# Kernel tuning notes

Hardware: AMD Instinct MI355X
Metric: run time of the kernel (lower is better)

The kernel has to match this reference:

```python
import jax, jax.numpy as jnp
import numpy as np

INF = 1e9
EPS = 1e-5

def layer_norm(x, g, b):
    mu = jnp.mean(x, axis=-1, keepdims=True)
    var = jnp.mean(jnp.square(x - mu), axis=-1, keepdims=True)
    return (x - mu) * jax.lax.rsqrt(var + EPS) * g + b

def setup_inputs() -> dict:
    key = jax.random.key(0)
    ks = jax.random.split(key, 12)
    B, S, N = 1, 512, 384
    c_in, c_hid, c_z, H = 64, 32, 128, 8
    d = c_hid * H
    sc = lambda fan: 1.0 / np.sqrt(fan)
    return {
        "m": jax.random.normal(ks[0], (B, S, N, c_in), jnp.float32),
        "z": jax.random.normal(ks[1], (B, N, N, c_z), jnp.float32),
        "mask": jnp.ones((B, N, N), jnp.float32),
        "gamma_m": jnp.ones((c_in,), jnp.float32),
        "beta_m": jnp.zeros((c_in,), jnp.float32),
        "gamma_z": jnp.ones((c_z,), jnp.float32),
        "beta_z": jnp.zeros((c_z,), jnp.float32),
        "w_z": jax.random.normal(ks[2], (c_z, H), jnp.float32) * sc(c_z),
        "b_z": jnp.zeros((H,), jnp.float32),
        "w_v": jax.random.normal(ks[3], (c_in, d), jnp.float32) * sc(c_in),
        "b_v": jnp.zeros((d,), jnp.float32),
        "w_g": jax.random.normal(ks[4], (c_in, d), jnp.float32) * sc(c_in),
        "b_g": jnp.zeros((d,), jnp.float32),
        "w_o": jax.random.normal(ks[5], (d, c_in), jnp.float32) * sc(d),
        "b_o": jnp.zeros((c_in,), jnp.float32),
    }

def reference(m, z, mask, gamma_m, beta_m, gamma_z, beta_z,
              w_z, b_z, w_v, b_v, w_g, b_g, w_o, b_o):
    B, S, N, c_in = m.shape
    H = w_z.shape[-1]
    C = w_v.shape[-1] // H
    # pair branch: LN -> linear -> [B,H,Nq,Nk] logits + mask bias -> softmax
    zn = layer_norm(z, gamma_z, beta_z)
    logits = jnp.einsum('bqkz,zh->bhqk', zn, w_z) + b_z[None, :, None, None]
    logits = logits + (INF * (mask - 1.0))[:, None, :, :]
    w = jax.nn.softmax(logits, axis=-1)                      # [B,H,Nq,Nk]
    # MSA branch: LN -> value / gate projections
    mn = layer_norm(m, gamma_m, beta_m)
    v = (mn @ w_v + b_v).reshape(B, S, N, H, C)              # [B,S,Nk,H,C]
    o = jnp.einsum('bhqk,bskhc->bsqhc', w, v)                # broadcast over S
    g = jax.nn.sigmoid(mn @ w_g + b_g).reshape(B, S, N, H, C)
    out = (o * g).reshape(B, S, N, H * C) @ w_o + b_o
    return out
```

## Files before the change

### kernel.cpp

```cpp
#include <hip/hip_runtime.h>
#include <hip/hip_bf16.h>

#define INFV 1e9f
#define EPSV 1e-5f

typedef unsigned short u16;
typedef unsigned int u32;
typedef __attribute__((ext_vector_type(8))) short short8;
typedef __attribute__((ext_vector_type(4))) float float4v;

__device__ __forceinline__ u16 f2us(float f) {
    u32 v;
    __builtin_memcpy(&v, &f, 4);
    u32 r = v + 0x7fffu + ((v >> 16) & 1u);
    return (u16)(r >> 16);
}

__device__ __forceinline__ float wred_sum(float x) {
    #pragma unroll
    for (int o = 32; o; o >>= 1) x += __shfl_xor(x, o);
    return x;
}
__device__ __forceinline__ float wred_max(float x) {
    #pragma unroll
    for (int o = 32; o; o >>= 1) x = fmaxf(x, __shfl_xor(x, o));
    return x;
}

__global__ __launch_bounds__(256) void k_prep_ln(
    const float* __restrict__ m, const float* __restrict__ gm, const float* __restrict__ bm,
    u16* __restrict__ mn,
    const float* __restrict__ wv, const float* __restrict__ wg,
    const float* __restrict__ wo, const float* __restrict__ wz,
    u16* __restrict__ wv_t, u16* __restrict__ wg_t,
    u16* __restrict__ wo_t, u16* __restrict__ wzT)
{
    if (blockIdx.x < 12288) {
        const int tid  = threadIdx.x;
        const int wid  = tid >> 6;
        const int lane = tid & 63;
        const int rloc = lane >> 4;
        const int c4   = (lane & 15) * 4;
        const int row  = blockIdx.x * 16 + wid * 4 + rloc;
        const float4 x = *(const float4*)(m + (size_t)row * 64 + c4);
        float s1 = x.x + x.y + x.z + x.w;
        float s2 = x.x * x.x + x.y * x.y + x.z * x.z + x.w * x.w;
        #pragma unroll
        for (int o = 8; o; o >>= 1) { s1 += __shfl_xor(s1, o); s2 += __shfl_xor(s2, o); }
        const float mean = s1 * (1.0f / 64.0f);
        const float var  = s2 * (1.0f / 64.0f) - mean * mean;
        const float rs   = rsqrtf(var + EPSV);
        const float4 g = *(const float4*)(gm + c4);
        const float4 b = *(const float4*)(bm + c4);
        uint2 pk;
        pk.x = (u32)f2us((x.x - mean) * rs * g.x + b.x) | ((u32)f2us((x.y - mean) * rs * g.y + b.y) << 16);
        pk.y = (u32)f2us((x.z - mean) * rs * g.z + b.z) | ((u32)f2us((x.w - mean) * rs * g.w + b.w) << 16);
        *(uint2*)(mn + (size_t)row * 64 + c4) = pk;
    } else {
        const int i = (blockIdx.x - 12288) * 256 + threadIdx.x;
        if (i < 16384) {
            const int n = i >> 6, k = i & 63;
            wv_t[i] = f2us(wv[(size_t)k * 256 + n]);
        } else if (i < 32768) {
            const int j = i - 16384, n = j >> 6, k = j & 63;
            wg_t[j] = f2us(wg[(size_t)k * 256 + n]);
        } else if (i < 49152) {
            const int j = i - 32768, n = j >> 8, k = j & 255;
            wo_t[j] = f2us(wo[(size_t)k * 64 + n]);
        } else if (i < 51200) {
            const int j = i - 49152, n = j >> 7, k = j & 127;
            wzT[j] = (n < 8) ? f2us(wz[(size_t)k * 8 + n]) : (u16)0;
        }
    }
}

__global__ __launch_bounds__(256) void k_vT(
    const u16* __restrict__ mn, const u16* __restrict__ wv_t, u16* __restrict__ vTf)
{
    const int tid  = threadIdx.x;
    const int wid  = tid >> 6;
    const int lane = tid & 63;
    const int lrow = lane & 15;
    const int lkg  = lane >> 4;
    const int s    = blockIdx.y;
    const int k0   = blockIdx.x * 64 + wid * 16;

    const int kt   = blockIdx.x * 2 + (wid >> 1);
    const int lkgc = (wid & 1) * 2 + (lkg >> 1);
    const int joff = (lkg & 1) * 4;

    const u16* mnk = mn + ((size_t)s * 384 + k0 + lrow) * 64;
    const short8 a0 = *(const short8*)(mnk + lkg * 8);
    const short8 a1 = *(const short8*)(mnk + 32 + lkg * 8);

    #pragma unroll
    for (int nt = 0; nt < 16; nt++) {
        const short8 b0 = *(const short8*)(wv_t + (size_t)(nt * 16 + lrow) * 64 + lkg * 8);
        const short8 b1 = *(const short8*)(wv_t + (size_t)(nt * 16 + lrow) * 64 + 32 + lkg * 8);
        float4v acc = (float4v){0.f, 0.f, 0.f, 0.f};
        acc = __builtin_amdgcn_mfma_f32_16x16x32_bf16(a0, b0, acc, 0, 0, 0);
        acc = __builtin_amdgcn_mfma_f32_16x16x32_bf16(a1, b1, acc, 0, 0, 0);
        uint2 pk;
        pk.x = (u32)f2us(acc[0]) | ((u32)f2us(acc[1]) << 16);
        pk.y = (u32)f2us(acc[2]) | ((u32)f2us(acc[3]) << 16);
        *(uint2*)(vTf + ((((size_t)s * 12 + kt) * 16 + nt) << 9)
                      + ((lkgc << 4) + lrow) * 8 + joff) = pk;
    }
}

__global__ __launch_bounds__(256) void k_logits2(
    const float* __restrict__ z, const float* __restrict__ mask,
    const float* __restrict__ gz, const float* __restrict__ bz,
    const u16* __restrict__ wzT, const float* __restrict__ bzb,
    float* __restrict__ wbuf)
{
    const int tid   = threadIdx.x;
    const int wid   = tid >> 6;
    const int lane  = tid & 63;
    const int lrow  = lane & 15;
    const int lkg   = lane >> 4;
    const int pair0 = (blockIdx.x * 4 + wid) * 16;

    float x[4][8];
    float s1 = 0.0f, s2 = 0.0f;
    #pragma unroll
    for (int ks = 0; ks < 4; ks++) {
        const float4* zp = (const float4*)(z + (size_t)(pair0 + lrow) * 128 + ks * 32 + lkg * 8);
        const float4 a = zp[0], b = zp[1];
        x[ks][0] = a.x; x[ks][1] = a.y; x[ks][2] = a.z; x[ks][3] = a.w;
        x[ks][4] = b.x; x[ks][5] = b.y; x[ks][6] = b.z; x[ks][7] = b.w;
        #pragma unroll
        for (int j = 0; j < 8; j++) { s1 += x[ks][j]; s2 += x[ks][j] * x[ks][j]; }
    }
    s1 += __shfl_xor(s1, 16); s1 += __shfl_xor(s1, 32);
    s2 += __shfl_xor(s2, 16); s2 += __shfl_xor(s2, 32);
    const float mean = s1 * (1.0f / 128.0f);
    const float var  = s2 * (1.0f / 128.0f) - mean * mean;
    const float rs   = rsqrtf(var + EPSV);

    float4v acc = (float4v){0.f, 0.f, 0.f, 0.f};
    #pragma unroll
    for (int ks = 0; ks < 4; ks++) {
        const int c0 = ks * 32 + lkg * 8;
        const float4 g0 = *(const float4*)(gz + c0);
        const float4 g1 = *(const float4*)(gz + c0 + 4);
        const float4 b0 = *(const float4*)(bz + c0);
        const float4 b1 = *(const float4*)(bz + c0 + 4);
        const float gv[8] = {g0.x, g0.y, g0.z, g0.w, g1.x, g1.y, g1.z, g1.w};
        const float bvv[8] = {b0.x, b0.y, b0.z, b0.w, b1.x, b1.y, b1.z, b1.w};
        short8 afr;
        #pragma unroll
        for (int j = 0; j < 8; j++)
            afr[j] = (short)f2us((x[ks][j] - mean) * rs * gv[j] + bvv[j]);
        const short8 bfr = *(const short8*)(wzT + (size_t)lrow * 128 + c0);
        acc = __builtin_amdgcn_mfma_f32_16x16x32_bf16(afr, bfr, acc, 0, 0, 0);
    }
    if (lrow < 8) {
        const float bzv = bzb[lrow];
        #pragma unroll
        for (int r = 0; r < 4; r++) {
            const int p = pair0 + lkg * 4 + r;
            const float mb = INFV * (mask[p] - 1.0f);
            wbuf[(size_t)lrow * 147456 + p] = acc[r] + bzv + mb;
        }
    }
}

__global__ __launch_bounds__(256) void k_softmax_f(
    const float* __restrict__ wbuf, u16* __restrict__ wbf)
{
    const int r = blockIdx.x * 4 + (threadIdx.x >> 6);
    const int lane = threadIdx.x & 63;
    const float* base = wbuf + (size_t)r * 384;
    float v[6];
    float mx = -1e30f;
    #pragma unroll
    for (int j = 0; j < 6; j++) {
        v[j] = base[lane + j * 64];
        mx = fmaxf(mx, v[j]);
    }
    mx = wred_max(mx);
    float s = 0.0f;
    #pragma unroll
    for (int j = 0; j < 6; j++) {
        v[j] = __expf(v[j] - mx);
        s += v[j];
    }
    s = wred_sum(s);
    const float inv = 1.0f / s;

    const int h  = r / 384;
    const int q  = r - h * 384;
    const int qb = q >> 5;
    const int mt = (q >> 4) & 1;
    const int lr = q & 15;
    #pragma unroll
    for (int j = 0; j < 6; j++) {
        const int k   = lane + j * 64;
        const int kt  = k >> 5;
        const int lkg = (k >> 3) & 3;
        const int jj  = k & 7;
        wbf[((((size_t)(qb * 8 + h) * 12 + kt) * 2 + mt) << 9) + ((lkg << 4) + lr) * 8 + jj]
            = f2us(v[j] * inv);
    }
}

__global__ __launch_bounds__(256) void k_softmax(
    const float* __restrict__ wbuf, u16* __restrict__ wb16)
{
    const int r = blockIdx.x * 4 + (threadIdx.x >> 6);
    const int lane = threadIdx.x & 63;
    const float* base = wbuf + (size_t)r * 384;
    float v[6];
    float mx = -1e30f;
    #pragma unroll
    for (int j = 0; j < 6; j++) {
        v[j] = base[lane + j * 64];
        mx = fmaxf(mx, v[j]);
    }
    mx = wred_max(mx);
    float s = 0.0f;
    #pragma unroll
    for (int j = 0; j < 6; j++) {
        v[j] = __expf(v[j] - mx);
        s += v[j];
    }
    s = wred_sum(s);
    const float inv = 1.0f / s;
    u16* ob = wb16 + (size_t)r * 384;
    #pragma unroll
    for (int j = 0; j < 6; j++) ob[lane + j * 64] = f2us(v[j] * inv);
}

__global__ __launch_bounds__(512, 4) void k_fused7(
    const u16* __restrict__ mn, const u16* __restrict__ vTf,
    const float* __restrict__ bv, const float* __restrict__ bg, const float* __restrict__ bo,
    const u16* __restrict__ wg_t, const u16* __restrict__ wo_t,
    const u16* __restrict__ wbf, float* __restrict__ out)
{
    __shared__ __align__(16) u16 og[128 * 264];

    const int tid  = threadIdx.x;
    const int w    = tid >> 6;
    const int wq   = w >> 1;
    const int wh   = w & 1;
    const int lane = tid & 63;
    const int lrow = lane & 15;
    const int lkg  = lane >> 4;

    const int bid  = blockIdx.x;
    const int xcd  = bid & 7;
    const int slot = bid >> 3;
    const int sdiv = slot / 3;
    const int q0   = (slot - sdiv * 3) * 128;
    const int s    = sdiv * 8 + xcd;

    const int qb = (q0 >> 5) + wq;

    float4v oacc[16];
    #pragma unroll
    for (int mt = 0; mt < 2; mt++)
        #pragma unroll
        for (int nt = 0; nt < 8; nt++) {
            const float b = bv[wh * 128 + nt * 16 + lrow];
            oacc[mt * 8 + nt] = (float4v){b, b, b, b};
        }

    for (int kt = 0; kt < 12; kt++) {
        short8 bb[8];
        #pragma unroll
        for (int nt = 0; nt < 8; nt++) {
            const int ntg = wh * 8 + nt;
            bb[nt] = *(const short8*)(vTf + ((((size_t)s * 12 + kt) * 16 + ntg) << 9) + lane * 8);
        }
        #pragma unroll
        for (int hl = 0; hl < 4; hl++) {
            const int h = wh * 4 + hl;
            const size_t abase = (((size_t)(qb * 8 + h) * 12 + kt) * 2) << 9;
            const short8 a0 = *(const short8*)(wbf + abase + lane * 8);
            const short8 a1 = *(const short8*)(wbf + abase + 512 + lane * 8);
            #pragma unroll
            for (int sub = 0; sub < 2; sub++) {
                const int nt = hl * 2 + sub;
                oacc[nt]     = __builtin_amdgcn_mfma_f32_16x16x32_bf16(a0, bb[nt], oacc[nt], 0, 0, 0);
                oacc[8 + nt] = __builtin_amdgcn_mfma_f32_16x16x32_bf16(a1, bb[nt], oacc[8 + nt], 0, 0, 0);
            }
        }
    }

    {
        const u16* mnq = mn + ((size_t)s * 384 + q0 + wq * 32 + lrow) * 64;
        #pragma unroll
        for (int mt = 0; mt < 2; mt++) {
            const short8 a0 = *(const short8*)(mnq + mt * 1024 + lkg * 8);
            const short8 a1 = *(const short8*)(mnq + mt * 1024 + 32 + lkg * 8);
            #pragma unroll
            for (int nt = 0; nt < 8; nt++) {
                const int hc0 = wh * 128 + nt * 16;
                const float bgv = bg[hc0 + lrow];
                const short8 b0 = *(const short8*)(wg_t + (size_t)(hc0 + lrow) * 64 + lkg * 8);
                const short8 b1 = *(const short8*)(wg_t + (size_t)(hc0 + lrow) * 64 + 32 + lkg * 8);
                float4v gacc = (float4v){bgv, bgv, bgv, bgv};
                gacc = __builtin_amdgcn_mfma_f32_16x16x32_bf16(a0, b0, gacc, 0, 0, 0);
                gacc = __builtin_amdgcn_mfma_f32_16x16x32_bf16(a1, b1, gacc, 0, 0, 0);
                #pragma unroll
                for (int r = 0; r < 4; r++) {
                    const float sg = 1.0f / (1.0f + __expf(-gacc[r]));
                    og[(size_t)(wq * 32 + mt * 16 + lkg * 4 + r) * 264 + hc0 + lrow]
                        = f2us(oacc[mt * 8 + nt][r] * sg);
                }
            }
        }
    }
    __syncthreads();

    #pragma unroll
    for (int mt = 0; mt < 2; mt++) {
        short8 af[8];
        #pragma unroll
        for (int ks = 0; ks < 8; ks++)
            af[ks] = *(const short8*)&og[(size_t)(wq * 32 + mt * 16 + lrow) * 264 + ks * 32 + lkg * 8];
        #pragma unroll
        for (int ntl = 0; ntl < 2; ntl++) {
            const int nto = wh * 2 + ntl;
            const float bov = bo[nto * 16 + lrow];
            float4v fac = (float4v){bov, bov, bov, bov};
            #pragma unroll
            for (int ks = 0; ks < 8; ks++) {
                const short8 b = *(const short8*)(wo_t + (size_t)(nto * 16 + lrow) * 256 + ks * 32 + lkg * 8);
                fac = __builtin_amdgcn_mfma_f32_16x16x32_bf16(af[ks], b, fac, 0, 0, 0);
            }
            #pragma unroll
            for (int r = 0; r < 4; r++)
                out[((size_t)s * 384 + q0 + wq * 32 + mt * 16 + lkg * 4 + r) * 64 + nto * 16 + lrow]
                    = fac[r];
        }
    }
}

__global__ __launch_bounds__(256, 2) void k_fused4(
    const u16* __restrict__ mn,
    const float* __restrict__ bv, const float* __restrict__ bg, const float* __restrict__ bo,
    const u16* __restrict__ wv_t, const u16* __restrict__ wg_t, const u16* __restrict__ wo_t,
    const u16* __restrict__ wb16, float* __restrict__ out)
{
    __shared__ __align__(16) char smem[67584];
    u16* vtt = (u16*)smem;
    u16* og  = (u16*)smem;

    const int tid  = threadIdx.x;
    const int wid  = tid >> 6;
    const int lane = tid & 63;
    const int lrow = lane & 15;
    const int lkg  = lane >> 4;
    const int s    = blockIdx.y;
    const int q0   = blockIdx.x * 128;

    const int vmt  = wid & 1;
    const int vnt0 = (wid >> 1) * 8;

    float4v oacc[32];
    #pragma unroll
    for (int mt = 0; mt < 2; mt++)
        #pragma unroll
        for (int nt = 0; nt < 16; nt++) {
            const float b = bv[nt * 16 + lrow];
            oacc[mt * 16 + nt] = (float4v){b, b, b, b};
        }

    for (int kt = 0; kt < 12; kt++) {
        const int k0 = kt * 32;
        float4v vacc[8];
        #pragma unroll
        for (int nt = 0; nt < 8; nt++) vacc[nt] = (float4v){0.f, 0.f, 0.f, 0.f};
        const u16* mnk = mn + ((size_t)s * 384 + k0 + vmt * 16 + lrow) * 64;
        #pragma unroll
        for (int ks = 0; ks < 2; ks++) {
            const short8 a = *(const short8*)(mnk + ks * 32 + lkg * 8);
            #pragma unroll
            for (int nt = 0; nt < 8; nt++) {
                const short8 b = *(const short8*)(wv_t + (size_t)((vnt0 + nt) * 16 + lrow) * 64 + ks * 32 + lkg * 8);
                vacc[nt] = __builtin_amdgcn_mfma_f32_16x16x32_bf16(a, b, vacc[nt], 0, 0, 0);
            }
        }
        u16* vb = vtt + (size_t)(kt & 1) * 8192;
        const int kg8 = vmt * 2 + (lkg >> 1);
        const int ko  = (lkg & 1) * 4;
        #pragma unroll
        for (int nt = 0; nt < 8; nt++) {
            uint2 pk;
            pk.x = (u32)f2us(vacc[nt][0]) | ((u32)f2us(vacc[nt][1]) << 16);
            pk.y = (u32)f2us(vacc[nt][2]) | ((u32)f2us(vacc[nt][3]) << 16);
            *(uint2*)&vb[((size_t)kg8 * 256 + (vnt0 + nt) * 16 + lrow) * 8 + ko] = pk;
        }
        __syncthreads();

        short8 ah[2][8];
        #pragma unroll
        for (int mt = 0; mt < 2; mt++)
            #pragma unroll
            for (int h = 0; h < 8; h++)
                ah[mt][h] = *(const short8*)(wb16 + (size_t)h * 147456
                              + (size_t)(q0 + wid * 32 + mt * 16 + lrow) * 384 + k0 + lkg * 8);
        #pragma unroll
        for (int nt = 0; nt < 16; nt++) {
            const short8 b = *(const short8*)&vb[((size_t)lkg * 256 + nt * 16 + lrow) * 8];
            oacc[nt]      = __builtin_amdgcn_mfma_f32_16x16x32_bf16(ah[0][nt >> 1], b, oacc[nt], 0, 0, 0);
            oacc[16 + nt] = __builtin_amdgcn_mfma_f32_16x16x32_bf16(ah[1][nt >> 1], b, oacc[16 + nt], 0, 0, 0);
        }
    }
    __syncthreads();

    #pragma unroll
    for (int mt = 0; mt < 2; mt++) {
        const u16* mnq = mn + ((size_t)s * 384 + q0 + wid * 32 + mt * 16 + lrow) * 64;
        const short8 a0 = *(const short8*)(mnq + lkg * 8);
        const short8 a1 = *(const short8*)(mnq + 32 + lkg * 8);
        #pragma unroll
        for (int nt = 0; nt < 16; nt++) {
            const float bgv = bg[nt * 16 + lrow];
            float4v gacc = (float4v){bgv, bgv, bgv, bgv};
            const short8 b0 = *(const short8*)(wg_t + (size_t)(nt * 16 + lrow) * 64 + lkg * 8);
            const short8 b1 = *(const short8*)(wg_t + (size_t)(nt * 16 + lrow) * 64 + 32 + lkg * 8);
            gacc = __builtin_amdgcn_mfma_f32_16x16x32_bf16(a0, b0, gacc, 0, 0, 0);
            gacc = __builtin_amdgcn_mfma_f32_16x16x32_bf16(a1, b1, gacc, 0, 0, 0);
            #pragma unroll
            for (int r = 0; r < 4; r++) {
                const float sg = 1.0f / (1.0f + __expf(-gacc[r]));
                og[(size_t)(wid * 32 + mt * 16 + lkg * 4 + r) * 264 + nt * 16 + lrow]
                    = f2us(oacc[mt * 16 + nt][r] * sg);
            }
        }
    }
    __syncthreads();

    #pragma unroll
    for (int mt = 0; mt < 2; mt++) {
        short8 af[8];
        #pragma unroll
        for (int ks = 0; ks < 8; ks++)
            af[ks] = *(const short8*)&og[(size_t)(wid * 32 + mt * 16 + lrow) * 264 + ks * 32 + lkg * 8];
        #pragma unroll
        for (int nt = 0; nt < 4; nt++) {
            const float bov = bo[nt * 16 + lrow];
            float4v fac = (float4v){bov, bov, bov, bov};
            #pragma unroll
            for (int ks = 0; ks < 8; ks++) {
                const short8 b = *(const short8*)(wo_t + (size_t)(nt * 16 + lrow) * 256 + ks * 32 + lkg * 8);
                fac = __builtin_amdgcn_mfma_f32_16x16x32_bf16(af[ks], b, fac, 0, 0, 0);
            }
            #pragma unroll
            for (int r = 0; r < 4; r++)
                out[((size_t)s * 384 + q0 + wid * 32 + mt * 16 + lkg * 4 + r) * 64 + nt * 16 + lrow]
                    = fac[r];
        }
    }
}

extern "C" void kernel_launch(void* const* d_in, const int* in_sizes, int n_in,
                              void* d_out, int out_size, void* d_ws, size_t ws_size,
                              hipStream_t stream) {
    const float* m    = (const float*)d_in[0];
    const float* z    = (const float*)d_in[1];
    const float* mask = (const float*)d_in[2];
    const float* gm   = (const float*)d_in[3];
    const float* bm   = (const float*)d_in[4];
    const float* gz   = (const float*)d_in[5];
    const float* bz   = (const float*)d_in[6];
    const float* wz   = (const float*)d_in[7];
    const float* bzb  = (const float*)d_in[8];
    const float* wv   = (const float*)d_in[9];
    const float* bv   = (const float*)d_in[10];
    const float* wg   = (const float*)d_in[11];
    const float* bg   = (const float*)d_in[12];
    const float* wo   = (const float*)d_in[13];
    const float* bo   = (const float*)d_in[14];
    float* out = (float*)d_out;

    char* ws = (char*)d_ws;
    float* wbuf = (float*)ws;
    u16*  wb16  = (u16*)(ws + 4718592);
    u16*  mn    = (u16*)(ws + 7077888);
    u16*  wv_t  = (u16*)(ws + 32243712);
    u16*  wg_t  = (u16*)(ws + 32276480);
    u16*  wo_t  = (u16*)(ws + 32309248);
    u16*  wzT   = (u16*)(ws + 32342016);
    u16*  vTf   = (u16*)(ws + 32346112);

    const bool big = ws_size >= 133009408ull;

    k_prep_ln<<<12488, 256, 0, stream>>>(m, gm, bm, mn, wv, wg, wo, wz, wv_t, wg_t, wo_t, wzT);
    if (big)
        k_vT<<<dim3(6, 512), 256, 0, stream>>>(mn, wv_t, vTf);
    k_logits2<<<2304, 256, 0, stream>>>(z, mask, gz, bz, wzT, bzb, wbuf);
    if (big) {
        k_softmax_f<<<768, 256, 0, stream>>>(wbuf, wb16);
        k_fused7<<<1536, 512, 0, stream>>>(mn, vTf, bv, bg, bo, wg_t, wo_t, wb16, out);
    } else {
        k_softmax<<<768, 256, 0, stream>>>(wbuf, wb16);
        k_fused4<<<dim3(3, 512), 256, 0, stream>>>(mn, bv, bg, bo, wv_t, wg_t, wo_t, wb16, out);
    }
}
```

Baseline: 422.4 us.

## Double-buffer V tiles in LDS via direct global-to-LDS loads in fused kernel

Instead of each wave loading its eight V B-fragments straight from global memory every k-step, the block cooperatively stages the next k-tile of V into a double-buffered LDS region using global_load_lds, then reads fragments from LDS. This shares V loads across the four q-waves that previously each fetched the same data, and overlaps the next tile's fetch with the current MFMAs. The cost is a __syncthreads per k-step and a larger shared footprint (67.5 KB, aliased with the output staging buffer), which may limit occupancy under the 4-blocks launch bound.

```diff
diff --git a/kernel.cpp b/kernel.cpp
--- a/kernel.cpp
+++ b/kernel.cpp
@@ -25,6 +25,13 @@
     #pragma unroll
     for (int o = 32; o; o >>= 1) x = fmaxf(x, __shfl_xor(x, o));
     return x;
+}
+
+__device__ __forceinline__ void gld16(const void* g, void* l) {
+    __builtin_amdgcn_global_load_lds(
+        (const __attribute__((address_space(1))) unsigned int*)g,
+        (__attribute__((address_space(3))) unsigned int*)l,
+        16, 0, 0);
 }
 
 __global__ __launch_bounds__(256) void k_prep_ln(
@@ -232,13 +239,15 @@
     for (int j = 0; j < 6; j++) ob[lane + j * 64] = f2us(v[j] * inv);
 }
 
-__global__ __launch_bounds__(512, 4) void k_fused7(
+__global__ __launch_bounds__(512, 4) void k_fused8(
     const u16* __restrict__ mn, const u16* __restrict__ vTf,
     const float* __restrict__ bv, const float* __restrict__ bg, const float* __restrict__ bo,
     const u16* __restrict__ wg_t, const u16* __restrict__ wo_t,
     const u16* __restrict__ wbf, float* __restrict__ out)
 {
-    __shared__ __align__(16) u16 og[128 * 264];
+    __shared__ __align__(16) char smem[67584];
+    u16* vtt = (u16*)smem;
+    u16* og  = (u16*)smem;
 
     const int tid  = threadIdx.x;
     const int w    = tid >> 6;
@@ -247,6 +256,7 @@
     const int lane = tid & 63;
     const int lrow = lane & 15;
     const int lkg  = lane >> 4;
+    const int stg  = w * 2;
 
     const int bid  = blockIdx.x;
     const int xcd  = bid & 7;
@@ -266,26 +276,39 @@
             oacc[mt * 8 + nt] = (float4v){b, b, b, b};
         }
 
+    const u16* vfs = vTf + (((size_t)s * 12) << 13);
+
+    {
+        const u16* gp = vfs + ((size_t)stg << 9) + lane * 8;
+        u16* lp = vtt + stg * 512;
+        gld16(gp, lp);
+        gld16(gp + 512, lp + 512);
+    }
+    __syncthreads();
+
     for (int kt = 0; kt < 12; kt++) {
-        short8 bb[8];
-        #pragma unroll
-        for (int nt = 0; nt < 8; nt++) {
-            const int ntg = wh * 8 + nt;
-            bb[nt] = *(const short8*)(vTf + ((((size_t)s * 12 + kt) * 16 + ntg) << 9) + lane * 8);
-        }
+        const int cur = kt & 1;
+        if (kt < 11) {
+            const u16* gp = vfs + ((((size_t)(kt + 1) * 16) + stg) << 9) + lane * 8;
+            u16* lp = vtt + (((cur ^ 1) * 16 + stg) * 512);
+            gld16(gp, lp);
+            gld16(gp + 512, lp + 512);
+        }
+        const u16* vb = vtt + cur * 8192;
         #pragma unroll
         for (int hl = 0; hl < 4; hl++) {
-            const int h = wh * 4 + hl;
-            const size_t abase = (((size_t)(qb * 8 + h) * 12 + kt) * 2) << 9;
+            const size_t abase = (((size_t)(qb * 8 + wh * 4 + hl) * 12 + kt) * 2) << 9;
             const short8 a0 = *(const short8*)(wbf + abase + lane * 8);
             const short8 a1 = *(const short8*)(wbf + abase + 512 + lane * 8);
-            #pragma unroll
-            for (int sub = 0; sub < 2; sub++) {
-                const int nt = hl * 2 + sub;
-                oacc[nt]     = __builtin_amdgcn_mfma_f32_16x16x32_bf16(a0, bb[nt], oacc[nt], 0, 0, 0);
-                oacc[8 + nt] = __builtin_amdgcn_mfma_f32_16x16x32_bf16(a1, bb[nt], oacc[8 + nt], 0, 0, 0);
-            }
-        }
+            const short8 b0 = *(const short8*)(vb + ((wh * 8 + hl * 2) * 512) + lane * 8);
+            const short8 b1 = *(const short8*)(vb + ((wh * 8 + hl * 2 + 1) * 512) + lane * 8);
+            const int nt = hl * 2;
+            oacc[nt]         = __builtin_amdgcn_mfma_f32_16x16x32_bf16(a0, b0, oacc[nt], 0, 0, 0);
+            oacc[8 + nt]     = __builtin_amdgcn_mfma_f32_16x16x32_bf16(a1, b0, oacc[8 + nt], 0, 0, 0);
+            oacc[nt + 1]     = __builtin_amdgcn_mfma_f32_16x16x32_bf16(a0, b1, oacc[nt + 1], 0, 0, 0);
+            oacc[8 + nt + 1] = __builtin_amdgcn_mfma_f32_16x16x32_bf16(a1, b1, oacc[8 + nt + 1], 0, 0, 0);
+        }
+        __syncthreads();
     }
 
     {
@@ -495,7 +518,7 @@
     k_logits2<<<2304, 256, 0, stream>>>(z, mask, gz, bz, wzT, bzb, wbuf);
     if (big) {
         k_softmax_f<<<768, 256, 0, stream>>>(wbuf, wb16);
-        k_fused7<<<1536, 512, 0, stream>>>(mn, vTf, bv, bg, bo, wg_t, wo_t, wb16, out);
+        k_fused8<<<1536, 512, 0, stream>>>(mn, vTf, bv, bg, bo, wg_t, wo_t, wb16, out);
     } else {
         k_softmax<<<768, 256, 0, stream>>>(wbuf, wb16);
         k_fused4<<<dim3(3, 512), 256, 0, stream>>>(mn, bv, bg, bo, wv_t, wg_t, wo_t, wb16, out);
```

New measurement: 389.2 us. 1.09x faster.
